# Optimization experiments

Measured on AMD Instinct MI355X. Metric: run time of the kernel, lower is better.

## Reference

```python
import jax, jax.numpy as jnp
import numpy as np


def setup_inputs() -> dict:
    key = jax.random.key(0)
    ks = jax.random.split(key, 5)
    B, S, D, H, dk = 4, 2048, 1024, 16, 64
    s = 0.02
    return {
        "x": jax.random.normal(ks[0], (B, S, D), dtype=jnp.float32),
        "Wq": jax.random.normal(ks[1], (H, D, dk), dtype=jnp.float32) * s,
        "Wk": jax.random.normal(ks[2], (H, D, dk), dtype=jnp.float32) * s,
        "Wv": jax.random.normal(ks[3], (H, D, dk), dtype=jnp.float32) * s,
        "Wo": jax.random.normal(ks[4], (H * dk, D), dtype=jnp.float32) * s,
    }


def reference(x, Wq, Wk, Wv, Wo):
    # Per-head projections: [B,S,D] x [H,D,dk] -> [B,H,S,dk]
    Q = jnp.einsum("bsd,hdk->bhsk", x, Wq)
    K = jnp.einsum("bsd,hdk->bhsk", x, Wk)
    V = jnp.einsum("bsd,hdk->bhsk", x, Wv)
    scale = 1.0 / jnp.sqrt(jnp.asarray(Wq.shape[-1], x.dtype))
    scores = jnp.einsum("bhqk,bhsk->bhqs", Q, K) * scale  # [B,H,S,S]
    attn = jax.nn.softmax(scores, axis=-1)
    out = jnp.einsum("bhqs,bhsk->bhqk", attn, V)  # [B,H,S,dk]
    B, H, S, dk = out.shape
    # concat heads along feature dim (matches torch.cat over head outputs)
    out = out.transpose(0, 2, 1, 3).reshape(B, S, H * dk)
    return out @ Wo  # [B,S,D]
```

## Files before the change

### kernel.cpp

```cpp
#include <hip/hip_runtime.h>
#include <hip/hip_bf16.h>
#include <stdint.h>

typedef __attribute__((ext_vector_type(8))) short bf16x8;
typedef __attribute__((ext_vector_type(4))) float f32x4;
typedef __attribute__((ext_vector_type(4))) unsigned short us4;

#define AS1C(p) ((const __attribute__((address_space(1))) void*)(p))
#define AS3(p)  ((__attribute__((address_space(3))) void*)(p))

#if __has_builtin(__builtin_amdgcn_exp2f)
#define EXP2(x) __builtin_amdgcn_exp2f(x)
#else
#define EXP2(x) __expf((x) * 0.69314718f)
#endif

#define MAX3(a,b,c) fmaxf(fmaxf((a),(b)),(c))

static __device__ __forceinline__ unsigned short f2b(float f) {
  union { __hip_bfloat16 h; unsigned short u; } cv;
  cv.h = __float2bfloat16(f);
  return cv.u;
}

static __device__ __forceinline__ unsigned int cvtpk(float a, float b) {
  unsigned int r;
  asm("v_cvt_pk_bf16_f32 %0, %1, %2" : "=v"(r) : "v"(a), "v"(b));
  return r;
}

__global__ __launch_bounds__(256) void conv_all_kernel(
    const float* __restrict__ x,  unsigned short* __restrict__ xb,
    const float* __restrict__ Wq, const float* __restrict__ Wk,
    const float* __restrict__ Wv, unsigned short* __restrict__ WqkvT,
    const float* __restrict__ Wo, unsigned short* __restrict__ WoT) {
  __shared__ float tile[64][65];
  const int bid = blockIdx.x;
  const int t = threadIdx.x;

  if (bid < 8192) {
    int i = bid * 256 + t;
    float4 v = ((const float4*)x)[i];
    us4 r = { f2b(v.x), f2b(v.y), f2b(v.z), f2b(v.w) };
    *(us4*)&xb[(size_t)i * 4] = r;
    return;
  }

  const int c  = t & 63;
  const int r0 = t >> 6;

  if (bid < 8960) {
    int b2 = bid - 8192;
    int which = b2 >> 8;
    int h  = (b2 >> 4) & 15;
    int dt = b2 & 15;
    const float* W = (which == 0) ? Wq : (which == 1 ? Wk : Wv);
    const float* src = W + (size_t)h * 65536 + (size_t)dt * 64 * 64;
#pragma unroll
    for (int it = 0; it < 16; ++it) {
      int r = r0 + it * 4;
      tile[r][c] = src[r * 64 + c];
    }
    __syncthreads();
    const size_t n0 = (size_t)which * 1024 + h * 64;
    const int d0 = dt * 64;
#pragma unroll
    for (int it = 0; it < 16; ++it) {
      int cc = r0 + it * 4;
      WqkvT[(n0 + cc) * 1024 + d0 + c] = f2b(tile[c][cc]);
    }
    return;
  }

  {
    int b2 = bid - 8960;
    int kt = b2 >> 4, nt = b2 & 15;
    const float* src = Wo + (size_t)(kt * 64) * 1024 + nt * 64;
#pragma unroll
    for (int it = 0; it < 16; ++it) {
      int r = r0 + it * 4;
      tile[r][c] = src[(size_t)r * 1024 + c];
    }
    __syncthreads();
#pragma unroll
    for (int it = 0; it < 16; ++it) {
      int cc = r0 + it * 4;
      WoT[((size_t)nt * 64 + cc) * 1024 + kt * 64 + c] = f2b(tile[c][cc]);
    }
  }
}

__global__ __launch_bounds__(512) void gemm_qkv_kernel(
    const unsigned short* __restrict__ A,
    const unsigned short* __restrict__ Bt,
    unsigned short* __restrict__ Q,
    unsigned short* __restrict__ Ko,
    unsigned short* __restrict__ Vt) {
  __shared__ __align__(16) unsigned short sA[128 * 32];
  __shared__ __align__(16) unsigned short sB[128 * 32];
  const int tid  = threadIdx.x;
  const int lane = tid & 63;
  const int wid  = tid >> 6;
  const int l15 = lane & 15, hi = lane >> 4;
  const int wr = wid >> 1, wc = wid & 1;
  const int n0 = blockIdx.y * 24 + blockIdx.x;
  const int n1 = (n0 & 7) * 192 + (n0 >> 3);
  const int brow = (n1 / 24) * 128;
  const int bcol = (n1 % 24) * 128;
  const int K = 1024;

  f32x4 acc[2][4] = {};

  const int r4 = tid >> 2;
  const int c8 = (tid & 3) * 8;
  const unsigned short* ga = A  + (size_t)(brow + r4) * K + c8;
  const unsigned short* gb = Bt + (size_t)(bcol + r4) * K + c8;
  unsigned short* lAw = sA + wid * 512;
  unsigned short* lBw = sB + wid * 512;

  for (int kb = 0; kb < K; kb += 32) {
    if (kb) __syncthreads();
    __builtin_amdgcn_global_load_lds(AS1C(ga + kb), AS3(lAw), 16, 0, 0);
    __builtin_amdgcn_global_load_lds(AS1C(gb + kb), AS3(lBw), 16, 0, 0);
    __syncthreads();

    bf16x8 af[2], bfr[4];
#pragma unroll
    for (int mi = 0; mi < 2; ++mi)
      af[mi] = *(const bf16x8*)&sA[(wr * 32 + mi * 16 + l15) * 32 + hi * 8];
#pragma unroll
    for (int ni = 0; ni < 4; ++ni)
      bfr[ni] = *(const bf16x8*)&sB[(wc * 64 + ni * 16 + l15) * 32 + hi * 8];
#pragma unroll
    for (int mi = 0; mi < 2; ++mi)
#pragma unroll
      for (int ni = 0; ni < 4; ++ni)
        acc[mi][ni] = __builtin_amdgcn_mfma_f32_16x16x32_bf16(af[mi], bfr[ni], acc[mi][ni], 0, 0, 0);
  }

#pragma unroll
  for (int mi = 0; mi < 2; ++mi) {
    int row0 = brow + wr * 32 + mi * 16 + hi * 4;
    int b = row0 >> 11, s0 = row0 & 2047;
#pragma unroll
    for (int ni = 0; ni < 4; ++ni) {
      int col = bcol + wc * 64 + ni * 16 + l15;
      int which = col >> 10;
      int h  = (col >> 6) & 15;
      int kk = col & 63;
      if (which == 2) {
        us4 pk = { f2b(acc[mi][ni][0]), f2b(acc[mi][ni][1]),
                   f2b(acc[mi][ni][2]), f2b(acc[mi][ni][3]) };
        *(us4*)&Vt[((size_t)(b * 16 + h) * 64 + kk) * 2048 + s0] = pk;
      } else {
        unsigned short* dst = (which == 0) ? Q : Ko;
        float scl = (which == 0) ? 0.18033688f : 1.0f;
#pragma unroll
        for (int j = 0; j < 4; ++j)
          dst[((size_t)(b * 16 + h) * 2048 + (s0 + j)) * 64 + kk] = f2b(acc[mi][ni][j] * scl);
      }
    }
  }
}

__global__ __launch_bounds__(512) void gemm_out_kernel(
    const unsigned short* __restrict__ A,
    const unsigned short* __restrict__ Bt,
    float* __restrict__ out) {
  __shared__ __align__(16) unsigned short sA[128 * 32];
  __shared__ __align__(16) unsigned short sB[128 * 32];
  const int tid  = threadIdx.x;
  const int lane = tid & 63;
  const int wid  = tid >> 6;
  const int l15 = lane & 15, hi = lane >> 4;
  const int wr = wid >> 1, wc = wid & 1;
  const int n0 = blockIdx.y * 8 + blockIdx.x;
  const int n1 = (n0 & 7) * 64 + (n0 >> 3);
  const int brow = (n1 >> 3) * 128;
  const int bcol = (n1 & 7) * 128;
  const int K = 1024;

  f32x4 acc[2][4] = {};

  const int r4 = tid >> 2;
  const int c8 = (tid & 3) * 8;
  const unsigned short* ga = A  + (size_t)(brow + r4) * K + c8;
  const unsigned short* gb = Bt + (size_t)(bcol + r4) * K + c8;
  unsigned short* lAw = sA + wid * 512;
  unsigned short* lBw = sB + wid * 512;

  for (int kb = 0; kb < K; kb += 32) {
    if (kb) __syncthreads();
    __builtin_amdgcn_global_load_lds(AS1C(ga + kb), AS3(lAw), 16, 0, 0);
    __builtin_amdgcn_global_load_lds(AS1C(gb + kb), AS3(lBw), 16, 0, 0);
    __syncthreads();

    bf16x8 af[2], bfr[4];
#pragma unroll
    for (int mi = 0; mi < 2; ++mi)
      af[mi] = *(const bf16x8*)&sA[(wr * 32 + mi * 16 + l15) * 32 + hi * 8];
#pragma unroll
    for (int ni = 0; ni < 4; ++ni)
      bfr[ni] = *(const bf16x8*)&sB[(wc * 64 + ni * 16 + l15) * 32 + hi * 8];
#pragma unroll
    for (int mi = 0; mi < 2; ++mi)
#pragma unroll
      for (int ni = 0; ni < 4; ++ni)
        acc[mi][ni] = __builtin_amdgcn_mfma_f32_16x16x32_bf16(af[mi], bfr[ni], acc[mi][ni], 0, 0, 0);
  }

#pragma unroll
  for (int mi = 0; mi < 2; ++mi) {
    int row0 = brow + wr * 32 + mi * 16 + hi * 4;
#pragma unroll
    for (int ni = 0; ni < 4; ++ni) {
      int col = bcol + wc * 64 + ni * 16 + l15;
#pragma unroll
      for (int j = 0; j < 4; ++j)
        out[(size_t)(row0 + j) * 1024 + col] = acc[mi][ni][j];
    }
  }
}

__global__ __launch_bounds__(512) void attn_kernel(
    const unsigned short* __restrict__ Q,
    const unsigned short* __restrict__ K,
    const unsigned short* __restrict__ Vt,
    unsigned short* __restrict__ O) {
  __shared__ __align__(16) unsigned short sK[2][64 * 64];
  __shared__ __align__(16) unsigned short sVt[2][64 * 64];
  __shared__ __align__(16) unsigned short sP[16][16 * 72];

  const int tid = threadIdx.x, lane = tid & 63, w = tid >> 6;
  const int l15 = lane & 15, hi = lane >> 4;
  const int n = blockIdx.x + (blockIdx.y << 3);
  const int bh = (n & 7) * 8 + (n >> 6);
  const int qx = (n >> 3) & 7;
  const int qb = qx * 256;
  const unsigned short* Qp  = Q  + (size_t)bh * 131072;
  const unsigned short* Kp  = K  + (size_t)bh * 131072;
  const unsigned short* Vtp = Vt + (size_t)bh * 131072;

  bf16x8 qf[2][2];
#pragma unroll
  for (int mi = 0; mi < 2; ++mi) {
    int qrow = qb + w * 32 + mi * 16 + l15;
    qf[mi][0] = *(const bf16x8*)&Qp[(size_t)qrow * 64 + hi * 8];
    qf[mi][1] = *(const bf16x8*)&Qp[(size_t)qrow * 64 + 32 + hi * 8];
  }

  bf16x8 ones;
#pragma unroll
  for (int j = 0; j < 8; ++j) ones[j] = (short)0x3F80;

  f32x4 o[2][4] = {};
  f32x4 lacc[2] = {};
  float m_[2] = { 0.f, 0.f };

  const int lrow = lane >> 3;
  const int uch  = (lane & 7) ^ lrow;
  const unsigned short* kg = Kp  + (size_t)(w * 8 + lrow) * 64   + uch * 8;
  const unsigned short* vg = Vtp + (size_t)(w * 8 + lrow) * 2048 + uch * 8;
  unsigned short* dK0 = &sK[0][w * 512];
  unsigned short* dK1 = &sK[1][w * 512];
  unsigned short* dV0 = &sVt[0][w * 512];
  unsigned short* dV1 = &sVt[1][w * 512];

  const int x7 = l15 & 7;
  const int ck0 = (hi ^ x7) * 8;
  const int ck1 = ((hi + 4) ^ x7) * 8;

  __builtin_amdgcn_global_load_lds(AS1C(kg), AS3(dK0), 16, 0, 0);
  __builtin_amdgcn_global_load_lds(AS1C(vg), AS3(dV0), 16, 0, 0);
  __syncthreads();

  for (int kt = 0; kt < 32; ++kt) {
    const int cur = kt & 1;
    if (kt < 31) {
      kg += 4096; vg += 64;
      __builtin_amdgcn_global_load_lds(AS1C(kg), AS3(cur ? dK0 : dK1), 16, 0, 0);
      __builtin_amdgcn_global_load_lds(AS1C(vg), AS3(cur ? dV0 : dV1), 16, 0, 0);
    }
    const unsigned short* sKc  = &sK[cur][0];
    const unsigned short* sVtc = &sVt[cur][0];

#pragma unroll
    for (int mi = 0; mi < 2; ++mi) {
      const float mneg = -m_[mi];
      f32x4 sc[4] = { { mneg, mneg, mneg, mneg }, { mneg, mneg, mneg, mneg },
                      { mneg, mneg, mneg, mneg }, { mneg, mneg, mneg, mneg } };
      __builtin_amdgcn_s_setprio(1);
#pragma unroll
      for (int ni = 0; ni < 4; ++ni) {
        bf16x8 kf0 = *(const bf16x8*)&sKc[(ni * 16 + l15) * 64 + ck0];
        bf16x8 kf1 = *(const bf16x8*)&sKc[(ni * 16 + l15) * 64 + ck1];
        sc[ni] = __builtin_amdgcn_mfma_f32_16x16x32_bf16(kf0, qf[mi][0], sc[ni], 0, 0, 0);
        sc[ni] = __builtin_amdgcn_mfma_f32_16x16x32_bf16(kf1, qf[mi][1], sc[ni], 0, 0, 0);
      }
      __builtin_amdgcn_s_setprio(0);

      float t0 = MAX3(sc[0][0], sc[0][1], sc[0][2]);
      float t1 = MAX3(sc[0][3], sc[1][0], sc[1][1]);
      float t2 = MAX3(sc[1][2], sc[1][3], sc[2][0]);
      float t3 = MAX3(sc[2][1], sc[2][2], sc[2][3]);
      float t4 = MAX3(sc[3][0], sc[3][1], sc[3][2]);
      float pmax = fmaxf(MAX3(t0, t1, t2), MAX3(t3, t4, sc[3][3]));

      if (!__all(pmax <= 8.0f)) {
        pmax = fmaxf(pmax, __shfl_xor(pmax, 16));
        pmax = fmaxf(pmax, __shfl_xor(pmax, 32));
        float delta = fmaxf(pmax, 0.f);
#pragma unroll
        for (int j = 0; j < 4; ++j) {
          float dj = __shfl(delta, hi * 4 + j);
          float aj = EXP2(-dj);
          lacc[mi][j] *= aj;
#pragma unroll
          for (int ni = 0; ni < 4; ++ni) o[mi][ni][j] *= aj;
        }
#pragma unroll
        for (int ni = 0; ni < 4; ++ni)
#pragma unroll
          for (int r = 0; r < 4; ++r) sc[ni][r] -= delta;
        m_[mi] += delta;
      }

      f32x4 p4[4];
#pragma unroll
      for (int ni = 0; ni < 4; ++ni)
#pragma unroll
        for (int r = 0; r < 4; ++r)
          p4[ni][r] = EXP2(sc[ni][r]);

      unsigned short* pb = &sP[w * 2 + mi][l15 * 72];
#pragma unroll
      for (int ni = 0; ni < 4; ++ni) {
        uint2 pk = { cvtpk(p4[ni][0], p4[ni][1]), cvtpk(p4[ni][2], p4[ni][3]) };
        *(uint2*)&pb[ni * 16 + hi * 4] = pk;
      }
    }

    bf16x8 pa[2][2];
#pragma unroll
    for (int mi = 0; mi < 2; ++mi) {
      pa[mi][0] = *(const bf16x8*)&sP[w * 2 + mi][l15 * 72 + hi * 8];
      pa[mi][1] = *(const bf16x8*)&sP[w * 2 + mi][l15 * 72 + 32 + hi * 8];
    }
    __builtin_amdgcn_s_setprio(1);
#pragma unroll
    for (int mi = 0; mi < 2; ++mi) {
      lacc[mi] = __builtin_amdgcn_mfma_f32_16x16x32_bf16(pa[mi][0], ones, lacc[mi], 0, 0, 0);
      lacc[mi] = __builtin_amdgcn_mfma_f32_16x16x32_bf16(pa[mi][1], ones, lacc[mi], 0, 0, 0);
    }
#pragma unroll
    for (int ni = 0; ni < 4; ++ni) {
      bf16x8 vf0 = *(const bf16x8*)&sVtc[(ni * 16 + l15) * 64 + ck0];
      bf16x8 vf1 = *(const bf16x8*)&sVtc[(ni * 16 + l15) * 64 + ck1];
#pragma unroll
      for (int mi = 0; mi < 2; ++mi) {
        o[mi][ni] = __builtin_amdgcn_mfma_f32_16x16x32_bf16(pa[mi][0], vf0, o[mi][ni], 0, 0, 0);
        o[mi][ni] = __builtin_amdgcn_mfma_f32_16x16x32_bf16(pa[mi][1], vf1, o[mi][ni], 0, 0, 0);
      }
    }
    __builtin_amdgcn_s_setprio(0);

    __syncthreads();
  }

  const int b = bh >> 4, h = bh & 15;
#pragma unroll
  for (int mi = 0; mi < 2; ++mi) {
#pragma unroll
    for (int j = 0; j < 4; ++j) {
      float inv = 1.0f / lacc[mi][j];
      int row = qb + w * 32 + mi * 16 + hi * 4 + j;
#pragma unroll
      for (int ni = 0; ni < 4; ++ni)
        O[((size_t)b * 2048 + row) * 1024 + h * 64 + ni * 16 + l15] = f2b(o[mi][ni][j] * inv);
    }
  }
}

extern "C" void kernel_launch(void* const* d_in, const int* in_sizes, int n_in,
                              void* d_out, int out_size, void* d_ws, size_t ws_size,
                              hipStream_t stream) {
  const float* x  = (const float*)d_in[0];
  const float* Wq = (const float*)d_in[1];
  const float* Wk = (const float*)d_in[2];
  const float* Wv = (const float*)d_in[3];
  const float* Wo = (const float*)d_in[4];
  float* out = (float*)d_out;

  char* w = (char*)d_ws;
  unsigned short* xb   = (unsigned short*)(w);
  unsigned short* wqkv = (unsigned short*)(w + 16777216);
  unsigned short* wo   = (unsigned short*)(w + 23068672);
  unsigned short* Qb   = (unsigned short*)(w + 25165824);
  unsigned short* Kb   = (unsigned short*)(w + 41943040);
  unsigned short* Vtb  = (unsigned short*)(w + 58720256);
  unsigned short* Ob   = (unsigned short*)(w + 75497472);

  conv_all_kernel<<<9216, 256, 0, stream>>>(x, xb, Wq, Wk, Wv, wqkv, Wo, wo);
  gemm_qkv_kernel<<<dim3(24, 64), 512, 0, stream>>>(xb, wqkv, Qb, Kb, Vtb);
  attn_kernel<<<dim3(8, 64), 512, 0, stream>>>(Qb, Kb, Vtb, Ob);
  gemm_out_kernel<<<dim3(8, 64), 512, 0, stream>>>(Ob, wo, out);
}
```

Before: 182.2 us.

## Triple-buffer LDS prefetch with XOR swizzle in QKV and output GEMMs

Replaces the single-buffered load-then-compute loop in both projection GEMMs with a three-stage ring of LDS buffers. Global-to-LDS loads are issued two k-steps ahead and waited on with explicit vmcnt counters and a single barrier per step, so memory latency can overlap with MFMA work. It also XOR-swizzles the 16-byte chunk placement within rows to reduce LDS bank conflicts on fragment reads. LDS use per block grows from 16 KB to 48 KB, which may limit occupancy.

```diff
diff --git a/kernel.cpp b/kernel.cpp
--- a/kernel.cpp
+++ b/kernel.cpp
@@ -16,6 +16,12 @@
 #endif
 
 #define MAX3(a,b,c) fmaxf(fmaxf((a),(b)),(c))
+
+#define SBAR() __builtin_amdgcn_sched_barrier(0)
+#define BARRIER() { SBAR(); __builtin_amdgcn_s_barrier(); SBAR(); }
+#define WAIT_LGKM0() { asm volatile("s_waitcnt lgkmcnt(0)" ::: "memory"); SBAR(); }
+#define WAIT_VM2() { asm volatile("s_waitcnt vmcnt(2)" ::: "memory"); SBAR(); }
+#define WAIT_VM0() { asm volatile("s_waitcnt vmcnt(0)" ::: "memory"); SBAR(); }
 
 static __device__ __forceinline__ unsigned short f2b(float f) {
   union { __hip_bfloat16 h; unsigned short u; } cv;
@@ -96,8 +102,7 @@
     unsigned short* __restrict__ Q,
     unsigned short* __restrict__ Ko,
     unsigned short* __restrict__ Vt) {
-  __shared__ __align__(16) unsigned short sA[128 * 32];
-  __shared__ __align__(16) unsigned short sB[128 * 32];
+  __shared__ __align__(16) unsigned short sL[3 * 8192];
   const int tid  = threadIdx.x;
   const int lane = tid & 63;
   const int wid  = tid >> 6;
@@ -111,32 +116,46 @@
 
   f32x4 acc[2][4] = {};
 
-  const int r4 = tid >> 2;
-  const int c8 = (tid & 3) * 8;
-  const unsigned short* ga = A  + (size_t)(brow + r4) * K + c8;
-  const unsigned short* gb = Bt + (size_t)(bcol + r4) * K + c8;
-  unsigned short* lAw = sA + wid * 512;
-  unsigned short* lBw = sB + wid * 512;
-
-  for (int kb = 0; kb < K; kb += 32) {
-    if (kb) __syncthreads();
-    __builtin_amdgcn_global_load_lds(AS1C(ga + kb), AS3(lAw), 16, 0, 0);
-    __builtin_amdgcn_global_load_lds(AS1C(gb + kb), AS3(lBw), 16, 0, 0);
-    __syncthreads();
-
+  const int srow = tid >> 2;
+  const int suc  = (tid & 3) ^ ((srow >> 1) & 3);
+  const unsigned short* gaS = A  + (size_t)(brow + srow) * K + suc * 8;
+  const unsigned short* gbS = Bt + (size_t)(bcol + srow) * K + suc * 8;
+  const int wofs = wid * 512;
+
+  const int ck = (hi ^ ((l15 >> 1) & 3)) * 8;
+  const int arow0 = wr * 32 + l15;
+  const int brow0 = wc * 64 + l15;
+
+#define QKV_STAGE(u) { \
+    unsigned short* dst_ = sL + ((u) % 3) * 8192 + wofs; \
+    __builtin_amdgcn_global_load_lds(AS1C(gaS + (u) * 32), AS3(dst_), 16, 0, 0); \
+    __builtin_amdgcn_global_load_lds(AS1C(gbS + (u) * 32), AS3(dst_ + 4096), 16, 0, 0); \
+  }
+
+  QKV_STAGE(0); QKV_STAGE(1);
+  WAIT_VM2(); BARRIER();
+
+  for (int t = 0; t < 32; ++t) {
+    if (t < 30) QKV_STAGE(t + 2);
+    const unsigned short* sA_ = sL + (t % 3) * 8192;
+    const unsigned short* sB_ = sA_ + 4096;
     bf16x8 af[2], bfr[4];
 #pragma unroll
     for (int mi = 0; mi < 2; ++mi)
-      af[mi] = *(const bf16x8*)&sA[(wr * 32 + mi * 16 + l15) * 32 + hi * 8];
+      af[mi] = *(const bf16x8*)&sA_[(arow0 + mi * 16) * 32 + ck];
 #pragma unroll
     for (int ni = 0; ni < 4; ++ni)
-      bfr[ni] = *(const bf16x8*)&sB[(wc * 64 + ni * 16 + l15) * 32 + hi * 8];
+      bfr[ni] = *(const bf16x8*)&sB_[(brow0 + ni * 16) * 32 + ck];
+    WAIT_LGKM0();
 #pragma unroll
     for (int mi = 0; mi < 2; ++mi)
 #pragma unroll
       for (int ni = 0; ni < 4; ++ni)
         acc[mi][ni] = __builtin_amdgcn_mfma_f32_16x16x32_bf16(af[mi], bfr[ni], acc[mi][ni], 0, 0, 0);
-  }
+    if (t < 30) { WAIT_VM2(); } else { WAIT_VM0(); }
+    BARRIER();
+  }
+#undef QKV_STAGE
 
 #pragma unroll
   for (int mi = 0; mi < 2; ++mi) {
@@ -167,8 +186,7 @@
     const unsigned short* __restrict__ A,
     const unsigned short* __restrict__ Bt,
     float* __restrict__ out) {
-  __shared__ __align__(16) unsigned short sA[128 * 32];
-  __shared__ __align__(16) unsigned short sB[128 * 32];
+  __shared__ __align__(16) unsigned short sL[3 * 8192];
   const int tid  = threadIdx.x;
   const int lane = tid & 63;
   const int wid  = tid >> 6;
@@ -182,32 +200,46 @@
 
   f32x4 acc[2][4] = {};
 
-  const int r4 = tid >> 2;
-  const int c8 = (tid & 3) * 8;
-  const unsigned short* ga = A  + (size_t)(brow + r4) * K + c8;
-  const unsigned short* gb = Bt + (size_t)(bcol + r4) * K + c8;
-  unsigned short* lAw = sA + wid * 512;
-  unsigned short* lBw = sB + wid * 512;
-
-  for (int kb = 0; kb < K; kb += 32) {
-    if (kb) __syncthreads();
-    __builtin_amdgcn_global_load_lds(AS1C(ga + kb), AS3(lAw), 16, 0, 0);
-    __builtin_amdgcn_global_load_lds(AS1C(gb + kb), AS3(lBw), 16, 0, 0);
-    __syncthreads();
-
+  const int srow = tid >> 2;
+  const int suc  = (tid & 3) ^ ((srow >> 1) & 3);
+  const unsigned short* gaS = A  + (size_t)(brow + srow) * K + suc * 8;
+  const unsigned short* gbS = Bt + (size_t)(bcol + srow) * K + suc * 8;
+  const int wofs = wid * 512;
+
+  const int ck = (hi ^ ((l15 >> 1) & 3)) * 8;
+  const int arow0 = wr * 32 + l15;
+  const int brow0 = wc * 64 + l15;
+
+#define OUT_STAGE(u) { \
+    unsigned short* dst_ = sL + ((u) % 3) * 8192 + wofs; \
+    __builtin_amdgcn_global_load_lds(AS1C(gaS + (u) * 32), AS3(dst_), 16, 0, 0); \
+    __builtin_amdgcn_global_load_lds(AS1C(gbS + (u) * 32), AS3(dst_ + 4096), 16, 0, 0); \
+  }
+
+  OUT_STAGE(0); OUT_STAGE(1);
+  WAIT_VM2(); BARRIER();
+
+  for (int t = 0; t < 32; ++t) {
+    if (t < 30) OUT_STAGE(t + 2);
+    const unsigned short* sA_ = sL + (t % 3) * 8192;
+    const unsigned short* sB_ = sA_ + 4096;
     bf16x8 af[2], bfr[4];
 #pragma unroll
     for (int mi = 0; mi < 2; ++mi)
-      af[mi] = *(const bf16x8*)&sA[(wr * 32 + mi * 16 + l15) * 32 + hi * 8];
+      af[mi] = *(const bf16x8*)&sA_[(arow0 + mi * 16) * 32 + ck];
 #pragma unroll
     for (int ni = 0; ni < 4; ++ni)
-      bfr[ni] = *(const bf16x8*)&sB[(wc * 64 + ni * 16 + l15) * 32 + hi * 8];
+      bfr[ni] = *(const bf16x8*)&sB_[(brow0 + ni * 16) * 32 + ck];
+    WAIT_LGKM0();
 #pragma unroll
     for (int mi = 0; mi < 2; ++mi)
 #pragma unroll
       for (int ni = 0; ni < 4; ++ni)
         acc[mi][ni] = __builtin_amdgcn_mfma_f32_16x16x32_bf16(af[mi], bfr[ni], acc[mi][ni], 0, 0, 0);
-  }
+    if (t < 30) { WAIT_VM2(); } else { WAIT_VM0(); }
+    BARRIER();
+  }
+#undef OUT_STAGE
 
 #pragma unroll
   for (int mi = 0; mi < 2; ++mi) {
```

Result: no change. 180.4 us (-1.0%).
